# Optimization experiments

Hardware: AMD Instinct MI355X
Metric: run time of the kernel (lower is better)

## Reference

```python
import jax, jax.numpy as jnp
import numpy as np

N_NODES = 50000
N_EDGES = 800000
D_FEAT = 128
HIDDEN = 256
N_CLASSES = 2


def setup_inputs() -> dict:
    key = jax.random.key(0)
    ks = jax.random.split(key, 9)
    x = jax.random.normal(ks[0], (N_NODES, D_FEAT), dtype=jnp.float32)
    edge_index = jax.random.randint(ks[1], (2, N_EDGES), 0, N_NODES, dtype=jnp.int32)
    # SAGEConv params: lin_l (applied to aggregated neighbors), lin_r (root), bias
    s1 = 1.0 / np.sqrt(D_FEAT)
    s2 = 1.0 / np.sqrt(HIDDEN)
    W1l = jax.random.normal(ks[2], (D_FEAT, HIDDEN), dtype=jnp.float32) * s1
    W1r = jax.random.normal(ks[3], (D_FEAT, HIDDEN), dtype=jnp.float32) * s1
    b1 = jax.random.normal(ks[4], (HIDDEN,), dtype=jnp.float32) * s1
    W2l = jax.random.normal(ks[5], (HIDDEN, N_CLASSES), dtype=jnp.float32) * s2
    W2r = jax.random.normal(ks[6], (HIDDEN, N_CLASSES), dtype=jnp.float32) * s2
    b2 = jax.random.normal(ks[7], (N_CLASSES,), dtype=jnp.float32) * s2
    return {"x": x, "edge_index": edge_index, "W1l": W1l, "W1r": W1r,
            "b1": b1, "W2l": W2l, "W2r": W2r, "b2": b2}


def _sage_conv(x, src, dst, Wl, Wr, b):
    # mean-aggregate neighbor features x[src] into destination nodes
    n = x.shape[0]
    agg = jax.ops.segment_sum(x[src], dst, num_segments=n)  # [N, d]
    deg = jax.ops.segment_sum(jnp.ones((src.shape[0],), x.dtype), dst,
                              num_segments=n)
    mean = agg / jnp.maximum(deg, 1.0)[:, None]
    return mean @ Wl + x @ Wr + b


def reference(x, edge_index, W1l, W1r, b1, W2l, W2r, b2):
    src, dst = edge_index[0], edge_index[1]
    h = jax.nn.relu(_sage_conv(x, src, dst, W1l, W1r, b1))
    embeddings = h  # dropout is identity in eval mode
    out = jax.nn.sigmoid(_sage_conv(embeddings, src, dst, W2l, W2r, b2))
    return out, embeddings
```

## Files before the change

kernel.cpp:

```cpp
#include <hip/hip_runtime.h>
#include <math.h>

#define N_NODES 50000
#define N_EDGES 800000
#define D_FEAT 128
#define HIDDEN 256
#define NB_SCAN 196
#define GEMM_BLOCKS 1563

#define PREP_CVT_B 512
#define PREP_CNT_B 256
#define PREP_WF_B 64
#define FILL_B 512
#define AGG_B 2048

typedef __bf16 bf16x8 __attribute__((ext_vector_type(8)));
typedef float f32x4 __attribute__((ext_vector_type(4)));

__device__ __forceinline__ unsigned f2b(float f) {
    unsigned u = __builtin_bit_cast(unsigned, f);
    return (u + 0x7fff + ((u >> 16) & 1)) >> 16;
}

__global__ __launch_bounds__(256) void prep(
    const float* __restrict__ x, const int* __restrict__ dst,
    const float* __restrict__ W1l, const float* __restrict__ W1r,
    unsigned* __restrict__ xb, int* __restrict__ cnt,
    unsigned short* __restrict__ Wfrag) {
    int b = blockIdx.x;
    int t = threadIdx.x;
    if (b < PREP_CVT_B) {
        for (int g = b * 256 + t; g < 800000; g += PREP_CVT_B * 256) {
            float4 v0 = *(const float4*)(x + (size_t)g * 8);
            float4 v1 = *(const float4*)(x + (size_t)g * 8 + 4);
            uint4 o;
            o.x = f2b(v0.x) | (f2b(v0.y) << 16);
            o.y = f2b(v0.z) | (f2b(v0.w) << 16);
            o.z = f2b(v1.x) | (f2b(v1.y) << 16);
            o.w = f2b(v1.z) | (f2b(v1.w) << 16);
            int d = g >> 4;
            int j = (g & 15) << 2;
            *(uint4*)(xb + (size_t)d * 64 + j) = o;
        }
    } else if (b < PREP_CVT_B + PREP_CNT_B) {
        for (int e = (b - PREP_CVT_B) * 256 + t; e < N_EDGES; e += PREP_CNT_B * 256)
            atomicAdd(&cnt[dst[e]], 1);
    } else {
        for (int tt = (b - PREP_CVT_B - PREP_CNT_B) * 256 + t; tt < 65536;
             tt += PREP_WF_B * 256) {
            int j = tt & 7;
            int lane = (tt >> 3) & 63;
            int ks = (tt >> 9) & 7;
            int nt = tt >> 12;
            int k = ks * 32 + ((lane >> 4) << 3) + j;
            int n = (nt << 4) + (lane & 15);
            float v = (k < 128) ? W1l[k * 256 + n] : W1r[(k - 128) * 256 + n];
            Wfrag[tt] = (unsigned short)f2b(v);
        }
    }
}

__global__ void scan1(const int* __restrict__ cnt, int* __restrict__ bsum) {
    __shared__ int tmp[256];
    int t = threadIdx.x;
    int i = blockIdx.x * 256 + t;
    tmp[t] = (i < N_NODES) ? cnt[i] : 0;
    __syncthreads();
    for (int off = 128; off > 0; off >>= 1) {
        if (t < off) tmp[t] += tmp[t + off];
        __syncthreads();
    }
    if (t == 0) bsum[blockIdx.x] = tmp[0];
}

__global__ void scanB(const int* __restrict__ cnt, const int* __restrict__ bsum,
                      int* __restrict__ rowpos) {
    __shared__ int bs[256];
    __shared__ int tmp[256];
    int t = threadIdx.x;
    int b = blockIdx.x;
    bs[t] = (t < NB_SCAN) ? bsum[t] : 0;
    __syncthreads();
    for (int off = 1; off < 256; off <<= 1) {
        int y = (t >= off) ? bs[t - off] : 0;
        __syncthreads();
        bs[t] += y;
        __syncthreads();
    }
    int boff = (b == 0) ? 0 : bs[b - 1];
    int i = b * 256 + t;
    int v = (i < N_NODES) ? cnt[i] : 0;
    tmp[t] = v;
    __syncthreads();
    for (int off = 1; off < 256; off <<= 1) {
        int y = (t >= off) ? tmp[t - off] : 0;
        __syncthreads();
        tmp[t] += y;
        __syncthreads();
    }
    if (i < N_NODES) rowpos[i] = tmp[t] - v + boff;
}

__global__ __launch_bounds__(256) void fill_kernel(
    const int* __restrict__ src, const int* __restrict__ dst,
    int* __restrict__ rowpos, unsigned short* __restrict__ esrc) {
    for (int e = blockIdx.x * 256 + threadIdx.x; e < N_EDGES; e += FILL_B * 256) {
        int pos = atomicAdd(&rowpos[dst[e]], 1);
        esrc[pos] = (unsigned short)src[e];
    }
}

__global__ __launch_bounds__(256) void agg1(
    const unsigned* __restrict__ xb, unsigned* __restrict__ mb,
    const unsigned short* __restrict__ esrc,
    const int* __restrict__ rowend, const int* __restrict__ cnt) {
    int wid = (blockIdx.x * 256 + threadIdx.x) >> 6;
    int lane = threadIdx.x & 63;
    for (int d = wid; d < N_NODES; d += AGG_B * 4) {
        int end = rowend[d];
        int c = cnt[d];
        float a0 = 0.0f, a1 = 0.0f;
        for (int base = end - c; base < end; base += 64) {
            int m = end - base; if (m > 64) m = 64;
            int idx = base + lane;
            int e = (int)esrc[idx < end ? idx : end - 1];
            for (int j0 = 0; j0 < m; j0 += 8) {
#pragma unroll
                for (int j = 0; j < 8; j++) {
                    int ss = __shfl(e, j0 + j);
                    unsigned u = xb[(size_t)ss * 64 + lane];
                    float sc = (j0 + j < m) ? 1.0f : 0.0f;
                    a0 += sc * __builtin_bit_cast(float, u << 16);
                    a1 += sc * __builtin_bit_cast(float, u & 0xffff0000u);
                }
            }
        }
        float inv = 1.0f / fmaxf((float)c, 1.0f);
        mb[(size_t)d * 64 + lane] = f2b(a0 * inv) | (f2b(a1 * inv) << 16);
    }
}

__global__ __launch_bounds__(256) void gemm1ps(
    const unsigned* __restrict__ mb, const unsigned* __restrict__ xb,
    const unsigned short* __restrict__ Wfrag, const float* __restrict__ b1,
    const float* __restrict__ W2l, const float* __restrict__ W2r,
    const float* __restrict__ b2,
    float* __restrict__ h, float* __restrict__ p, float* __restrict__ s) {
    __shared__ unsigned A[32 * 128];
    __shared__ float ppart[32][4];

    int r0 = blockIdx.x * 32;
    int tid = threadIdx.x;
    int w = tid >> 6;
    int lane = tid & 63;
    int quad = lane >> 4;
    int l15 = lane & 15;

    if (tid < 128) ((float*)ppart)[tid] = 0.0f;

    int sr = tid >> 3;
    int c0 = tid & 7;
#pragma unroll
    for (int j = 0; j < 4; j++) {
        int c = c0 + (j << 3);
        uint4 v;
        if (c < 16) v = *(const uint4*)(mb + (size_t)(r0 + sr) * 64 + (c << 2));
        else        v = *(const uint4*)(xb + (size_t)(r0 + sr) * 64 + ((c - 16) << 2));
        int cp = c ^ (sr & 7);
        *(uint4*)(A + sr * 128 + (cp << 2)) = v;
    }
    __syncthreads();

    f32x4 acc[8];
#pragma unroll
    for (int i = 0; i < 8; i++) acc[i] = (f32x4){0.0f, 0.0f, 0.0f, 0.0f};

    for (int ks = 0; ks < 8; ks++) {
        bf16x8 bfr[4];
#pragma unroll
        for (int nt = 0; nt < 4; nt++) {
            int ntg = (w << 2) + nt;
            uint4 raw = *(const uint4*)(Wfrag + ((((ntg << 3) + ks) << 6) + lane) * 8);
            bfr[nt] = __builtin_bit_cast(bf16x8, raw);
        }
#pragma unroll
        for (int mt = 0; mt < 2; mt++) {
            int row = (mt << 4) + l15;
            int c = (ks << 2) + quad;
            uint4 araw = *(const uint4*)(A + row * 128 + ((c ^ (row & 7)) << 2));
            bf16x8 afr = __builtin_bit_cast(bf16x8, araw);
#pragma unroll
            for (int nt = 0; nt < 4; nt++) {
                acc[(mt << 2) + nt] = __builtin_amdgcn_mfma_f32_16x16x32_bf16(
                    afr, bfr[nt], acc[(mt << 2) + nt], 0, 0, 0);
            }
        }
    }

    float w2[4][4];
#pragma unroll
    for (int nt = 0; nt < 4; nt++) {
        int col = (w << 6) + (nt << 4) + l15;
        float2 l2 = *(const float2*)(W2l + col * 2);
        float2 r2 = *(const float2*)(W2r + col * 2);
        w2[nt][0] = l2.x; w2[nt][1] = l2.y; w2[nt][2] = r2.x; w2[nt][3] = r2.y;
    }

#pragma unroll
    for (int mt = 0; mt < 2; mt++) {
        float red[4][4];
#pragma unroll
        for (int v = 0; v < 4; v++)
#pragma unroll
            for (int r = 0; r < 4; r++) red[v][r] = 0.0f;

#pragma unroll
        for (int nt = 0; nt < 4; nt++) {
            int col = (w << 6) + (nt << 4) + l15;
            float b = b1[col];
            f32x4 v = acc[(mt << 2) + nt];
#pragma unroll
            for (int r = 0; r < 4; r++) {
                float hv = v[r] + b;
                hv = hv > 0.0f ? hv : 0.0f;
                int row = r0 + (mt << 4) + (quad << 2) + r;
                if (row < N_NODES)
                    __builtin_nontemporal_store(hv, &h[(size_t)row * 256 + col]);
                red[0][r] += hv * w2[nt][0];
                red[1][r] += hv * w2[nt][1];
                red[2][r] += hv * w2[nt][2];
                red[3][r] += hv * w2[nt][3];
            }
        }
#pragma unroll
        for (int v = 0; v < 4; v++)
#pragma unroll
            for (int r = 0; r < 4; r++) {
                red[v][r] += __shfl_xor(red[v][r], 1);
                red[v][r] += __shfl_xor(red[v][r], 2);
                red[v][r] += __shfl_xor(red[v][r], 4);
                red[v][r] += __shfl_xor(red[v][r], 8);
            }
        if (l15 == 0) {
            int lrow = (mt << 4) + (quad << 2);
#pragma unroll
            for (int r = 0; r < 4; r++)
#pragma unroll
                for (int v = 0; v < 4; v++)
                    atomicAdd(&ppart[lrow + r][v], red[v][r]);
        }
    }
    __syncthreads();

    if (tid < 32) {
        int row = r0 + tid;
        if (row < N_NODES) {
            float2 pv = {ppart[tid][0], ppart[tid][1]};
            float2 sv = {ppart[tid][2] + b2[0], ppart[tid][3] + b2[1]};
            *(float2*)(p + (size_t)row * 2) = pv;
            *(float2*)(s + (size_t)row * 2) = sv;
        }
    }
}

__global__ __launch_bounds__(256) void agg2(
    const float* __restrict__ p, const float* __restrict__ s,
    const unsigned short* __restrict__ esrc,
    const int* __restrict__ rowend, const int* __restrict__ cnt,
    float* __restrict__ out) {
    int wid = (blockIdx.x * 256 + threadIdx.x) >> 6;
    int lane = threadIdx.x & 63;
    for (int d = wid; d < N_NODES; d += AGG_B * 4) {
        int end = rowend[d];
        int c = cnt[d];
        float a0 = 0.0f, a1 = 0.0f;
        for (int base = end - c; base < end; base += 64) {
            int idx = base + lane;
            if (idx < end) {
                int ss = (int)esrc[idx];
                float2 v = *(const float2*)(p + (size_t)ss * 2);
                a0 += v.x; a1 += v.y;
            }
        }
#pragma unroll
        for (int off = 32; off > 0; off >>= 1) {
            a0 += __shfl_down(a0, off);
            a1 += __shfl_down(a1, off);
        }
        if (lane == 0) {
            float inv = 1.0f / fmaxf((float)c, 1.0f);
            float z0 = a0 * inv + s[(size_t)d * 2 + 0];
            float z1 = a1 * inv + s[(size_t)d * 2 + 1];
            float2 o = {1.0f / (1.0f + expf(-z0)), 1.0f / (1.0f + expf(-z1))};
            *(float2*)(out + (size_t)d * 2) = o;
        }
    }
}

extern "C" void kernel_launch(void* const* d_in, const int* in_sizes, int n_in,
                              void* d_out, int out_size, void* d_ws, size_t ws_size,
                              hipStream_t stream) {
    const float* x   = (const float*)d_in[0];
    const int*   ei  = (const int*)d_in[1];
    const float* W1l = (const float*)d_in[2];
    const float* W1r = (const float*)d_in[3];
    const float* b1  = (const float*)d_in[4];
    const float* W2l = (const float*)d_in[5];
    const float* W2r = (const float*)d_in[6];
    const float* b2  = (const float*)d_in[7];

    const int* src = ei;
    const int* dst = ei + N_EDGES;

    float* out = (float*)d_out;
    float* emb = out + (size_t)N_NODES * 2;

    int* cnt    = (int*)d_ws;
    int* rowpos = cnt + N_NODES;
    int* bsum   = rowpos + N_NODES;
    unsigned short* esrc = (unsigned short*)(bsum + 256);
    unsigned* xb = (unsigned*)(esrc + 800064);
    unsigned* mb = xb + (size_t)50048 * 64;
    unsigned short* Wfrag = (unsigned short*)(mb + (size_t)50048 * 64);
    float* p = (float*)(Wfrag + 65536);
    float* s = p + (size_t)N_NODES * 2;

    hipMemsetAsync(cnt, 0, N_NODES * sizeof(int), stream);

    prep<<<PREP_CVT_B + PREP_CNT_B + PREP_WF_B, 256, 0, stream>>>(
        x, dst, W1l, W1r, xb, cnt, Wfrag);

    scan1<<<NB_SCAN, 256, 0, stream>>>(cnt, bsum);
    scanB<<<NB_SCAN, 256, 0, stream>>>(cnt, bsum, rowpos);
    fill_kernel<<<FILL_B, 256, 0, stream>>>(src, dst, rowpos, esrc);

    agg1<<<AGG_B, 256, 0, stream>>>(xb, mb, esrc, rowpos, cnt);

    gemm1ps<<<GEMM_BLOCKS, 256, 0, stream>>>(mb, xb, Wfrag, b1, W2l, W2r, b2,
                                             emb, p, s);

    agg2<<<AGG_B, 256, 0, stream>>>(p, s, esrc, rowpos, cnt, out);
}
```

Before: 259.0 us.

## Build CSR with per-slice shared-memory histograms and partitioned scatter

Replaces the global-atomic degree count and global-atomic fill with a two-level counting sort. Each of 64 edge slices builds a packed 16-bit histogram in LDS, per-slice offsets are derived by a column scan, and a scatter pass uses LDS atomics over 8 node partitions. The intent is to remove contended global atomics and make the CSR order deterministic. The cost is extra kernels, a 64×N offset array written to and read back from global memory, and 8× redundant reads of the edge list in the scatter pass.

```diff
diff --git a/kernel.cpp b/kernel.cpp
--- a/kernel.cpp
+++ b/kernel.cpp
@@ -9,10 +9,13 @@
 #define GEMM_BLOCKS 1563
 
 #define PREP_CVT_B 512
-#define PREP_CNT_B 256
 #define PREP_WF_B 64
-#define FILL_B 512
 #define AGG_B 2048
+
+#define NSLICE 64
+#define SLICE_E 12500
+#define NPART 8
+#define PART_N 6250
 
 typedef __bf16 bf16x8 __attribute__((ext_vector_type(8)));
 typedef float f32x4 __attribute__((ext_vector_type(4)));
@@ -23,10 +26,9 @@
 }
 
 __global__ __launch_bounds__(256) void prep(
-    const float* __restrict__ x, const int* __restrict__ dst,
+    const float* __restrict__ x,
     const float* __restrict__ W1l, const float* __restrict__ W1r,
-    unsigned* __restrict__ xb, int* __restrict__ cnt,
-    unsigned short* __restrict__ Wfrag) {
+    unsigned* __restrict__ xb, unsigned short* __restrict__ Wfrag) {
     int b = blockIdx.x;
     int t = threadIdx.x;
     if (b < PREP_CVT_B) {
@@ -42,12 +44,8 @@
             int j = (g & 15) << 2;
             *(uint4*)(xb + (size_t)d * 64 + j) = o;
         }
-    } else if (b < PREP_CVT_B + PREP_CNT_B) {
-        for (int e = (b - PREP_CVT_B) * 256 + t; e < N_EDGES; e += PREP_CNT_B * 256)
-            atomicAdd(&cnt[dst[e]], 1);
     } else {
-        for (int tt = (b - PREP_CVT_B - PREP_CNT_B) * 256 + t; tt < 65536;
-             tt += PREP_WF_B * 256) {
+        for (int tt = (b - PREP_CVT_B) * 256 + t; tt < 65536; tt += PREP_WF_B * 256) {
             int j = tt & 7;
             int lane = (tt >> 3) & 63;
             int ks = (tt >> 9) & 7;
@@ -60,11 +58,34 @@
     }
 }
 
-__global__ void scan1(const int* __restrict__ cnt, int* __restrict__ bsum) {
+__global__ __launch_bounds__(256) void hist_kernel(const int* __restrict__ dst,
+                                                   unsigned* __restrict__ arr) {
+    __shared__ unsigned hist[25000];
+    int i = blockIdx.x;
+    int t = threadIdx.x;
+    for (int k = t; k < 25000; k += 256) hist[k] = 0;
+    __syncthreads();
+    int e0 = i * SLICE_E;
+    for (int k = t; k < SLICE_E; k += 256) {
+        int d = dst[e0 + k];
+        atomicAdd(&hist[d >> 1], (d & 1) ? 65536u : 1u);
+    }
+    __syncthreads();
+    for (int d = t; d < N_NODES; d += 256)
+        arr[(size_t)i * N_NODES + d] = (hist[d >> 1] >> ((d & 1) << 4)) & 0xffffu;
+}
+
+__global__ void scan1(const unsigned* __restrict__ arr, int* __restrict__ cnt,
+                      int* __restrict__ bsum) {
     __shared__ int tmp[256];
     int t = threadIdx.x;
     int i = blockIdx.x * 256 + t;
-    tmp[t] = (i < N_NODES) ? cnt[i] : 0;
+    int c = 0;
+    if (i < N_NODES) {
+        for (int k = 0; k < NSLICE; k++) c += (int)arr[(size_t)k * N_NODES + i];
+        cnt[i] = c;
+    }
+    tmp[t] = c;
     __syncthreads();
     for (int off = 128; off > 0; off >>= 1) {
         if (t < off) tmp[t] += tmp[t + off];
@@ -74,7 +95,7 @@
 }
 
 __global__ void scanB(const int* __restrict__ cnt, const int* __restrict__ bsum,
-                      int* __restrict__ rowpos) {
+                      int* __restrict__ rowbeg) {
     __shared__ int bs[256];
     __shared__ int tmp[256];
     int t = threadIdx.x;
@@ -98,29 +119,57 @@
         tmp[t] += y;
         __syncthreads();
     }
-    if (i < N_NODES) rowpos[i] = tmp[t] - v + boff;
-}
-
-__global__ __launch_bounds__(256) void fill_kernel(
+    if (i < N_NODES) rowbeg[i] = tmp[t] - v + boff;
+}
+
+__global__ __launch_bounds__(256) void offs_kernel(const int* __restrict__ rowbeg,
+                                                   unsigned* __restrict__ arr) {
+    int d = blockIdx.x * 256 + threadIdx.x;
+    if (d >= N_NODES) return;
+    unsigned running = (unsigned)rowbeg[d];
+#pragma unroll 4
+    for (int k = 0; k < NSLICE; k++) {
+        unsigned old = arr[(size_t)k * N_NODES + d];
+        arr[(size_t)k * N_NODES + d] = running;
+        running += old;
+    }
+}
+
+__global__ __launch_bounds__(256) void scatter_kernel(
     const int* __restrict__ src, const int* __restrict__ dst,
-    int* __restrict__ rowpos, unsigned short* __restrict__ esrc) {
-    for (int e = blockIdx.x * 256 + threadIdx.x; e < N_EDGES; e += FILL_B * 256) {
-        int pos = atomicAdd(&rowpos[dst[e]], 1);
-        esrc[pos] = (unsigned short)src[e];
+    const unsigned* __restrict__ arr, unsigned short* __restrict__ esrc) {
+    __shared__ unsigned off[PART_N];
+    int g = blockIdx.x & 7;
+    int i = blockIdx.x >> 3;
+    int t = threadIdx.x;
+    int lo = g * PART_N;
+    for (int k = t; k < PART_N; k += 256)
+        off[k] = arr[(size_t)i * N_NODES + lo + k];
+    __syncthreads();
+    int e0 = i * SLICE_E;
+    for (int k = t; k < SLICE_E; k += 256) {
+        int e = e0 + k;
+        int d = dst[e];
+        unsigned dl = (unsigned)(d - lo);
+        if (dl < (unsigned)PART_N) {
+            unsigned pos = atomicAdd(&off[dl], 1u);
+            esrc[pos] = (unsigned short)src[e];
+        }
     }
 }
 
 __global__ __launch_bounds__(256) void agg1(
     const unsigned* __restrict__ xb, unsigned* __restrict__ mb,
     const unsigned short* __restrict__ esrc,
-    const int* __restrict__ rowend, const int* __restrict__ cnt) {
+    const int* __restrict__ rowbeg, const int* __restrict__ cnt) {
     int wid = (blockIdx.x * 256 + threadIdx.x) >> 6;
     int lane = threadIdx.x & 63;
     for (int d = wid; d < N_NODES; d += AGG_B * 4) {
-        int end = rowend[d];
+        int beg = rowbeg[d];
         int c = cnt[d];
+        int end = beg + c;
         float a0 = 0.0f, a1 = 0.0f;
-        for (int base = end - c; base < end; base += 64) {
+        for (int base = beg; base < end; base += 64) {
             int m = end - base; if (m > 64) m = 64;
             int idx = base + lane;
             int e = (int)esrc[idx < end ? idx : end - 1];
@@ -266,15 +315,16 @@
 __global__ __launch_bounds__(256) void agg2(
     const float* __restrict__ p, const float* __restrict__ s,
     const unsigned short* __restrict__ esrc,
-    const int* __restrict__ rowend, const int* __restrict__ cnt,
+    const int* __restrict__ rowbeg, const int* __restrict__ cnt,
     float* __restrict__ out) {
     int wid = (blockIdx.x * 256 + threadIdx.x) >> 6;
     int lane = threadIdx.x & 63;
     for (int d = wid; d < N_NODES; d += AGG_B * 4) {
-        int end = rowend[d];
+        int beg = rowbeg[d];
         int c = cnt[d];
+        int end = beg + c;
         float a0 = 0.0f, a1 = 0.0f;
-        for (int base = end - c; base < end; base += 64) {
+        for (int base = beg; base < end; base += 64) {
             int idx = base + lane;
             if (idx < end) {
                 int ss = (int)esrc[idx];
@@ -316,28 +366,28 @@
     float* emb = out + (size_t)N_NODES * 2;
 
     int* cnt    = (int*)d_ws;
-    int* rowpos = cnt + N_NODES;
-    int* bsum   = rowpos + N_NODES;
+    int* rowbeg = cnt + N_NODES;
+    int* bsum   = rowbeg + N_NODES;
     unsigned short* esrc = (unsigned short*)(bsum + 256);
     unsigned* xb = (unsigned*)(esrc + 800064);
     unsigned* mb = xb + (size_t)50048 * 64;
+    unsigned* arr = mb;
     unsigned short* Wfrag = (unsigned short*)(mb + (size_t)50048 * 64);
     float* p = (float*)(Wfrag + 65536);
     float* s = p + (size_t)N_NODES * 2;
 
-    hipMemsetAsync(cnt, 0, N_NODES * sizeof(int), stream);
-
-    prep<<<PREP_CVT_B + PREP_CNT_B + PREP_WF_B, 256, 0, stream>>>(
-        x, dst, W1l, W1r, xb, cnt, Wfrag);
-
-    scan1<<<NB_SCAN, 256, 0, stream>>>(cnt, bsum);
-    scanB<<<NB_SCAN, 256, 0, stream>>>(cnt, bsum, rowpos);
-    fill_kernel<<<FILL_B, 256, 0, stream>>>(src, dst, rowpos, esrc);
-
-    agg1<<<AGG_B, 256, 0, stream>>>(xb, mb, esrc, rowpos, cnt);
+    prep<<<PREP_CVT_B + PREP_WF_B, 256, 0, stream>>>(x, W1l, W1r, xb, Wfrag);
+
+    hist_kernel<<<NSLICE, 256, 0, stream>>>(dst, arr);
+    scan1<<<NB_SCAN, 256, 0, stream>>>(arr, cnt, bsum);
+    scanB<<<NB_SCAN, 256, 0, stream>>>(cnt, bsum, rowbeg);
+    offs_kernel<<<NB_SCAN, 256, 0, stream>>>(rowbeg, arr);
+    scatter_kernel<<<NSLICE * NPART, 256, 0, stream>>>(src, dst, arr, esrc);
+
+    agg1<<<AGG_B, 256, 0, stream>>>(xb, mb, esrc, rowbeg, cnt);
 
     gemm1ps<<<GEMM_BLOCKS, 256, 0, stream>>>(mb, xb, Wfrag, b1, W2l, W2r, b2,
                                              emb, p, s);
 
-    agg2<<<AGG_B, 256, 0, stream>>>(p, s, esrc, rowpos, cnt, out);
-}
+    agg2<<<AGG_B, 256, 0, stream>>>(p, s, esrc, rowbeg, cnt, out);
+}
```

Measured after the change: 239.2 us. 7.7% less time.
